# Performance work log

Hardware: AMD Instinct MI355X
Metric: run time of the kernel (lower is better)

## Reference

```python
import jax, jax.numpy as jnp
import numpy as np

B, M, LSEQ, D, K, H, DFF, NL = 16, 512, 1024, 128, 16, 8, 512, 2


def layernorm(x, g, b):
    mu = x.mean(-1, keepdims=True)
    var = ((x - mu) ** 2).mean(-1, keepdims=True)
    return (x - mu) * jax.lax.rsqrt(var + 1e-5) * g + b


def gcn_conv(x, row, col, W, b, N):
    # PyG GCNConv: xW, add self-loops, symmetric D^-1/2 (A+I) D^-1/2 aggregation
    xw = x @ W
    loop = jnp.arange(N)
    row2 = jnp.concatenate([row, loop])
    col2 = jnp.concatenate([col, loop])
    deg = jax.ops.segment_sum(jnp.ones(row2.shape[0], xw.dtype), col2, num_segments=N)
    dinv = jnp.where(deg > 0, jax.lax.rsqrt(deg), 0.0)
    norm = dinv[row2] * dinv[col2]  # [E+N]
    out = jax.ops.segment_sum(norm[:, None] * xw[row2], col2, num_segments=N)
    return out + b


def encoder_layer(q, kv, Wq, Wk, Wv, Wo, ln1_g, ln1_b, W1, b1, W2, b2, ln2_g, ln2_b):
    Bb, Mq, d = q.shape
    dh = d // H
    qh = (q @ Wq).reshape(Bb, Mq, H, dh)
    kh = (kv @ Wk).reshape(Bb, -1, H, dh)
    vh = (kv @ Wv).reshape(Bb, -1, H, dh)
    scores = jnp.einsum('bqhd,bkhd->bhqk', qh, kh) / jnp.sqrt(jnp.float32(dh))
    attn = jax.nn.softmax(scores, axis=-1)
    o = jnp.einsum('bhqk,bkhd->bqhd', attn, vh).reshape(Bb, Mq, d) @ Wo
    x = layernorm(q + o, ln1_g, ln1_b)
    ff = jax.nn.relu(x @ W1 + b1) @ W2 + b2
    return layernorm(x + ff, ln2_g, ln2_b)


def setup_inputs() -> dict:
    key = jax.random.key(0)
    ks = jax.random.split(key, 24)
    s = 0.05
    return {
        'enc_out_vari': jax.random.normal(ks[0], (B, M, D), jnp.float32),
        'x_enc': jax.random.normal(ks[1], (B, LSEQ, M), jnp.float32),
        'gcn_w1': jax.random.normal(ks[2], (D, D), jnp.float32) * s,
        'gcn_b1': jnp.zeros((D,), jnp.float32),
        'gcn_w2': jax.random.normal(ks[3], (D, D), jnp.float32) * s,
        'gcn_b2': jnp.zeros((D,), jnp.float32),
        'Wq': jax.random.normal(ks[4], (NL, D, D), jnp.float32) * s,
        'Wk': jax.random.normal(ks[5], (NL, D, D), jnp.float32) * s,
        'Wv': jax.random.normal(ks[6], (NL, D, D), jnp.float32) * s,
        'Wo': jax.random.normal(ks[7], (NL, D, D), jnp.float32) * s,
        'ln1_g': jnp.ones((NL, D), jnp.float32),
        'ln1_b': jnp.zeros((NL, D), jnp.float32),
        'W1': jax.random.normal(ks[8], (NL, D, DFF), jnp.float32) * s,
        'b1': jnp.zeros((NL, DFF), jnp.float32),
        'W2': jax.random.normal(ks[9], (NL, DFF, D), jnp.float32) * s,
        'b2': jnp.zeros((NL, D), jnp.float32),
        'ln2_g': jnp.ones((NL, D), jnp.float32),
        'ln2_b': jnp.zeros((NL, D), jnp.float32),
    }


def reference(enc_out_vari, x_enc, gcn_w1, gcn_b1, gcn_w2, gcn_b2, Wq, Wk, Wv, Wo,
              ln1_g, ln1_b, W1, b1, W2, b2, ln2_g, ln2_b):
    Bb, Mm, d = enc_out_vari.shape
    # --- Pearson correlation kNN graph build (ascending argsort as in source) ---
    xt = x_enc.transpose(0, 2, 1)  # [B, M, L]
    c = xt - xt.mean(-1, keepdims=True)
    cov = jnp.einsum('bml,bnl->bmn', c, c) / jnp.float32(LSEQ - 1)
    std = jnp.sqrt(jnp.diagonal(cov, axis1=-2, axis2=-1))
    std = jnp.where(std == 0, 1.0, std)
    corr = cov / (std[:, :, None] * std[:, None, :])
    neighbors = jnp.argsort(corr, axis=-1)[:, :, 1:K + 1]  # [B, M, K]
    # rows tiled, cols node-major (faithful to source's repeat/reshape mismatch)
    row = jnp.tile(jnp.arange(Mm), K)[None, :]           # [1, M*K]
    col = neighbors.reshape(Bb, -1)                      # [B, M*K]
    offs = (jnp.arange(Bb) * Mm)[:, None]
    row_g = jnp.broadcast_to(row + offs, (Bb, Mm * K)).reshape(-1)
    col_g = (col + offs).reshape(-1)
    N = Bb * Mm
    # --- 2-layer GCN on the disjoint-union graph (dropout is identity in eval) ---
    x_raw = enc_out_vari.reshape(N, d)
    x1 = jax.nn.relu(gcn_conv(x_raw, row_g, col_g, gcn_w1, gcn_b1, N))
    x2 = jax.nn.relu(gcn_conv(x1, row_g, col_g, gcn_w2, gcn_b2, N))
    kv = x2.reshape(Bb, Mm, d)
    # --- Transformer encoder: enc_out_vari attends to GCN features ---
    h = enc_out_vari
    for l in range(NL):
        h = encoder_layer(h, kv, Wq[l], Wk[l], Wv[l], Wo[l], ln1_g[l], ln1_b[l],
                          W1[l], b1[l], W2[l], b2[l], ln2_g[l], ln2_b[l])
    return h
```

## Files before the change

### kernel.cpp

```cpp
#include <hip/hip_runtime.h>
#include <math.h>

#define BB 16
#define MM 512
#define LL 1024
#define DD 128
#define KK 16
#define HH 8
#define DHH 16
#define NDFF 512
#define NNODE (BB*MM)
#define NEDGE (NNODE*KK)

typedef __attribute__((ext_vector_type(8))) short bf16x8;
typedef __attribute__((ext_vector_type(4))) float f32x4;
#define MFMA(a,b,c) __builtin_amdgcn_mfma_f32_16x16x32_bf16(a,b,c,0,0,0)

__device__ inline unsigned short bf16rne(float x) {
  union { float f; unsigned u; } v; v.f = x;
  return (unsigned short)((v.u + 0x7FFFu + ((v.u >> 16) & 1u)) >> 16);
}
__device__ inline float bf16tof(unsigned short h) {
  union { unsigned u; float f; } v; v.u = ((unsigned)h) << 16; return v.f;
}
__device__ inline void hilo(float x, unsigned short& h, unsigned short& l) {
  h = bf16rne(x);
  l = bf16rne(x - bf16tof(h));
}

__device__ inline void async16(const void* g, void* l) {
  __builtin_amdgcn_global_load_lds(
      (const __attribute__((address_space(1))) unsigned int*)g,
      (__attribute__((address_space(3))) unsigned int*)l, 16, 0, 0);
}

__global__ __launch_bounds__(256) void transpose_x_kernel(const float* __restrict__ X,
                                                          unsigned short* __restrict__ XTh,
                                                          unsigned short* __restrict__ XTl) {
  __shared__ float t[32][33];
  int b = blockIdx.z;
  int m0 = blockIdx.x * 32, l0 = blockIdx.y * 32;
  int c = threadIdx.x & 31, r = threadIdx.x >> 5;
  const float* Xb = X + (size_t)b * LL * MM;
  #pragma unroll
  for (int i = 0; i < 4; ++i)
    t[r + i*8][c] = Xb[(size_t)(l0 + r + i*8) * MM + m0 + c];
  __syncthreads();
  int R = m0 >> 6;
  int rbase = m0 & 63;
  size_t base = ((size_t)(b * 8 + R)) * 65536 + (size_t)(l0 >> 5) * 2048
              + (size_t)(c >> 3) * 512 + (c & 7);
  #pragma unroll
  for (int i = 0; i < 4; ++i) {
    unsigned short h, l;
    hilo(t[c][r + i*8], h, l);
    size_t idx = base + (size_t)(rbase + r + i*8) * 8;
    XTh[idx] = h; XTl[idx] = l;
  }
}

__global__ __launch_bounds__(256) void transpose_w_kernel(
    const float* __restrict__ gw1, const float* __restrict__ gw2,
    const float* __restrict__ Wq, const float* __restrict__ Wk,
    const float* __restrict__ Wv, const float* __restrict__ Wo,
    const float* __restrict__ W1, const float* __restrict__ W2,
    unsigned short* __restrict__ wTh, unsigned short* __restrict__ wTl) {
  int z = blockIdx.z;
  const float* src; int K, N; size_t doff;
  if (z < 10) {
    K = 128; N = 128;
    switch (z) {
      case 0: src = gw1;         doff = 0;         break;
      case 1: src = gw2;         doff = 16384;     break;
      case 2: src = Wk;          doff = 2*16384;   break;
      case 3: src = Wv;          doff = 3*16384;   break;
      case 4: src = Wk + 16384;  doff = 4*16384;   break;
      case 5: src = Wv + 16384;  doff = 5*16384;   break;
      case 6: src = Wq;          doff = 6*16384;   break;
      case 7: src = Wq + 16384;  doff = 7*16384;   break;
      case 8: src = Wo;          doff = 8*16384;   break;
      default: src = Wo + 16384; doff = 9*16384;   break;
    }
  } else if (z < 12) {
    K = 128; N = 512; doff = 163840 + (size_t)(z - 10) * 65536;
    src = W1 + (size_t)(z - 10) * 65536;
  } else {
    K = 512; N = 128; doff = 294912 + (size_t)(z - 12) * 65536;
    src = W2 + (size_t)(z - 12) * 65536;
  }
  int k0 = blockIdx.x * 32, n0 = blockIdx.y * 32;
  if (k0 >= K || n0 >= N) return;
  __shared__ float t[32][33];
  int c = threadIdx.x & 31, r = threadIdx.x >> 5;
  #pragma unroll
  for (int i = 0; i < 4; ++i)
    t[r + i*8][c] = src[(size_t)(k0 + r + i*8) * N + n0 + c];
  __syncthreads();
  #pragma unroll
  for (int i = 0; i < 4; ++i) {
    size_t idx = doff + (size_t)(n0 + r + i*8) * K + k0 + c;
    unsigned short h, l;
    hilo(t[c][r + i*8], h, l);
    wTh[idx] = h; wTl[idx] = l;
  }
}

__global__ void split_kernel(const float* __restrict__ in,
                             unsigned short* __restrict__ h,
                             unsigned short* __restrict__ l) {
  int i = blockIdx.x * 256 + threadIdx.x;
  float4 v = ((const float4*)in)[i];
  unsigned short h0,h1,h2,h3,l0,l1,l2,l3;
  hilo(v.x,h0,l0); hilo(v.y,h1,l1); hilo(v.z,h2,l2); hilo(v.w,h3,l3);
  uint2 hh, ll;
  hh.x = (unsigned)h0 | ((unsigned)h1 << 16); hh.y = (unsigned)h2 | ((unsigned)h3 << 16);
  ll.x = (unsigned)l0 | ((unsigned)l1 << 16); ll.y = (unsigned)l2 | ((unsigned)l3 << 16);
  ((uint2*)h)[i] = hh; ((uint2*)l)[i] = ll;
}

__global__ void colmean_part_kernel(const float* __restrict__ X, float* __restrict__ part) {
  int bm = blockIdx.x * 256 + threadIdx.x;
  int b = bm >> 9, m = bm & (MM - 1);
  int l0 = blockIdx.y * 128;
  const float* p = X + (size_t)b * LL * MM + (size_t)l0 * MM + m;
  float s = 0.f;
  #pragma unroll 8
  for (int l = 0; l < 128; ++l) s += p[(size_t)l * MM];
  part[(size_t)blockIdx.y * NNODE + bm] = s;
}

__global__ void colmean_finish_kernel(const float* __restrict__ part, float* __restrict__ mu) {
  int bm = blockIdx.x * 256 + threadIdx.x;
  float s = 0.f;
  #pragma unroll
  for (int j = 0; j < 8; ++j) s += part[(size_t)j * NNODE + bm];
  mu[bm] = s * (1.f / 1024.f);
}

__global__ __launch_bounds__(256) void gram_kernel(const unsigned short* __restrict__ XTh,
                                                   const unsigned short* __restrict__ XTl,
                                                   float* __restrict__ G0,
                                                   float* __restrict__ G1) {
  __shared__ unsigned short lAh[2048], lAl[2048], lBh[2048], lBl[2048];
  int b = blockIdx.y, z = blockIdx.z;
  int pi = blockIdx.x;
  int ti = 0, rem = pi;
  while (rem >= 8 - ti) { rem -= 8 - ti; ++ti; }
  int tj = ti + rem;
  int tid = threadIdx.x;
  int wid = tid >> 6, lane = tid & 63;
  int wr = wid >> 1, wc = wid & 1;
  int fr = lane & 15, fkb = lane >> 4;
  size_t abase = ((size_t)(b * 8 + ti)) * 65536 + (size_t)z * 16 * 2048;
  size_t bbase = ((size_t)(b * 8 + tj)) * 65536 + (size_t)z * 16 * 2048;
  int toff = tid * 8;
  int aoff0 = fkb * 512 + (wr*32 + fr) * 8;
  int aoff1 = aoff0 + 128;
  int boff0 = fkb * 512 + (wc*32 + fr) * 8;
  int boff1 = boff0 + 128;
  f32x4 acc00 = {0,0,0,0}, acc01 = {0,0,0,0}, acc10 = {0,0,0,0}, acc11 = {0,0,0,0};
  for (int s = 0; s < 16; ++s) {
    size_t ao = abase + (size_t)s * 2048 + toff;
    size_t bo = bbase + (size_t)s * 2048 + toff;
    async16(XTh + ao, lAh + toff);
    async16(XTl + ao, lAl + toff);
    async16(XTh + bo, lBh + toff);
    async16(XTl + bo, lBl + toff);
    __syncthreads();
    bf16x8 a0h = *(const bf16x8*)(lAh + aoff0);
    bf16x8 a1h = *(const bf16x8*)(lAh + aoff1);
    bf16x8 a0l = *(const bf16x8*)(lAl + aoff0);
    bf16x8 a1l = *(const bf16x8*)(lAl + aoff1);
    bf16x8 b0h = *(const bf16x8*)(lBh + boff0);
    bf16x8 b1h = *(const bf16x8*)(lBh + boff1);
    bf16x8 b0l = *(const bf16x8*)(lBl + boff0);
    bf16x8 b1l = *(const bf16x8*)(lBl + boff1);
    acc00 = MFMA(a0h, b0h, acc00); acc00 = MFMA(a0h, b0l, acc00); acc00 = MFMA(a0l, b0h, acc00);
    acc01 = MFMA(a0h, b1h, acc01); acc01 = MFMA(a0h, b1l, acc01); acc01 = MFMA(a0l, b1h, acc01);
    acc10 = MFMA(a1h, b0h, acc10); acc10 = MFMA(a1h, b0l, acc10); acc10 = MFMA(a1l, b0h, acc10);
    acc11 = MFMA(a1h, b1h, acc11); acc11 = MFMA(a1h, b1l, acc11); acc11 = MFMA(a1l, b1h, acc11);
    __syncthreads();
  }
  int m0 = ti * 64, n0 = tj * 64;
  float* G = (z ? G1 : G0) + (size_t)b * MM * MM;
  int mirror = (ti != tj);
  #pragma unroll
  for (int i = 0; i < 2; ++i) {
    #pragma unroll
    for (int j = 0; j < 2; ++j) {
      const f32x4& a = (i == 0) ? (j == 0 ? acc00 : acc01) : (j == 0 ? acc10 : acc11);
      #pragma unroll
      for (int r = 0; r < 4; ++r) {
        int row = m0 + wr*32 + i*16 + (lane >> 4)*4 + r;
        int col = n0 + wc*32 + j*16 + (lane & 15);
        float v = a[r];
        G[(size_t)row * MM + col] = v;
        if (mirror) G[(size_t)col * MM + row] = v;
      }
    }
  }
}

__global__ __launch_bounds__(256) void bf_gemm_k128_kernel(
    const unsigned short* __restrict__ Ah, const unsigned short* __restrict__ Al,
    const unsigned short* __restrict__ Bh, const unsigned short* __restrict__ Bl,
    float* __restrict__ C, unsigned short* __restrict__ Ch, unsigned short* __restrict__ Cl,
    int Ldc, int col0, const float* __restrict__ bias,
    const float* __restrict__ resid, int relu) {
  int tid = threadIdx.x;
  int m0 = blockIdx.y * 64, n0 = blockIdx.x * 64;
  int wid = tid >> 6, lane = tid & 63;
  int wr = wid >> 1, wc = wid & 1;
  int fr = lane & 15, fkb = lane >> 4;
  size_t arow0 = (size_t)(m0 + wr*32 + fr) * 128;
  size_t arow1 = arow0 + 16 * 128;
  size_t brow0 = (size_t)(n0 + wc*32 + fr) * 128;
  size_t brow1 = brow0 + 16 * 128;
  bf16x8 fa0h[4], fa1h[4], fa0l[4], fa1l[4];
  bf16x8 fb0h[4], fb1h[4], fb0l[4], fb1l[4];
  #pragma unroll
  for (int ks = 0; ks < 4; ++ks) {
    int ko = ks * 32 + fkb * 8;
    fa0h[ks] = *(const bf16x8*)(Ah + arow0 + ko);
    fa1h[ks] = *(const bf16x8*)(Ah + arow1 + ko);
    fa0l[ks] = *(const bf16x8*)(Al + arow0 + ko);
    fa1l[ks] = *(const bf16x8*)(Al + arow1 + ko);
    fb0h[ks] = *(const bf16x8*)(Bh + brow0 + ko);
    fb1h[ks] = *(const bf16x8*)(Bh + brow1 + ko);
    fb0l[ks] = *(const bf16x8*)(Bl + brow0 + ko);
    fb1l[ks] = *(const bf16x8*)(Bl + brow1 + ko);
  }
  f32x4 acc00 = {0,0,0,0}, acc01 = {0,0,0,0}, acc10 = {0,0,0,0}, acc11 = {0,0,0,0};
  #pragma unroll
  for (int ks = 0; ks < 4; ++ks) {
    acc00 = MFMA(fa0h[ks], fb0h[ks], acc00);
    acc00 = MFMA(fa0h[ks], fb0l[ks], acc00);
    acc00 = MFMA(fa0l[ks], fb0h[ks], acc00);
    acc01 = MFMA(fa0h[ks], fb1h[ks], acc01);
    acc01 = MFMA(fa0h[ks], fb1l[ks], acc01);
    acc01 = MFMA(fa0l[ks], fb1h[ks], acc01);
    acc10 = MFMA(fa1h[ks], fb0h[ks], acc10);
    acc10 = MFMA(fa1h[ks], fb0l[ks], acc10);
    acc10 = MFMA(fa1l[ks], fb0h[ks], acc10);
    acc11 = MFMA(fa1h[ks], fb1h[ks], acc11);
    acc11 = MFMA(fa1h[ks], fb1l[ks], acc11);
    acc11 = MFMA(fa1l[ks], fb1h[ks], acc11);
  }
  #pragma unroll
  for (int i = 0; i < 2; ++i) {
    #pragma unroll
    for (int j = 0; j < 2; ++j) {
      const f32x4& a = (i == 0) ? (j == 0 ? acc00 : acc01) : (j == 0 ? acc10 : acc11);
      #pragma unroll
      for (int r = 0; r < 4; ++r) {
        int row = m0 + wr*32 + i*16 + (lane >> 4)*4 + r;
        int col = col0 + n0 + wc*32 + j*16 + (lane & 15);
        float v = a[r];
        if (bias)  v += bias[col - col0];
        if (resid) v += resid[(size_t)row * Ldc + col];
        if (relu)  v = fmaxf(v, 0.f);
        size_t o = (size_t)row * Ldc + col;
        if (C) C[o] = v;
        if (Ch) {
          unsigned short hh, ll;
          hilo(v, hh, ll);
          Ch[o] = hh; Cl[o] = ll;
        }
      }
    }
  }
}

__global__ __launch_bounds__(512) void bf_gemm_sk_kernel(
    const unsigned short* __restrict__ Ah, const unsigned short* __restrict__ Al,
    const unsigned short* __restrict__ Bh, const unsigned short* __restrict__ Bl,
    float* __restrict__ C, unsigned short* __restrict__ Ch, unsigned short* __restrict__ Cl,
    int Ldc, int col0, int Kd, const float* __restrict__ bias,
    const float* __restrict__ resid, int relu) {
  __shared__ float red[64][65];
  int tid = threadIdx.x;
  int m0 = blockIdx.y * 64, n0 = blockIdx.x * 64;
  int wid = tid >> 6, lane = tid & 63;
  int kg = wid >> 2;
  int w4 = wid & 3;
  int wr = w4 >> 1, wc = w4 & 1;
  int fr = lane & 15, fkb = lane >> 4;
  int Kh = Kd >> 1;
  size_t arow0 = (size_t)(m0 + wr*32 + fr) * Kd + (size_t)kg * Kh;
  size_t arow1 = arow0 + (size_t)16 * Kd;
  size_t brow0 = (size_t)(n0 + wc*32 + fr) * Kd + (size_t)kg * Kh;
  size_t brow1 = brow0 + (size_t)16 * Kd;
  f32x4 acc00 = {0,0,0,0}, acc01 = {0,0,0,0}, acc10 = {0,0,0,0}, acc11 = {0,0,0,0};
  int ko = fkb * 8;
  bf16x8 a0h = *(const bf16x8*)(Ah + arow0 + ko);
  bf16x8 a1h = *(const bf16x8*)(Ah + arow1 + ko);
  bf16x8 a0l = *(const bf16x8*)(Al + arow0 + ko);
  bf16x8 a1l = *(const bf16x8*)(Al + arow1 + ko);
  bf16x8 b0h = *(const bf16x8*)(Bh + brow0 + ko);
  bf16x8 b1h = *(const bf16x8*)(Bh + brow1 + ko);
  bf16x8 b0l = *(const bf16x8*)(Bl + brow0 + ko);
  bf16x8 b1l = *(const bf16x8*)(Bl + brow1 + ko);
  for (int k0 = 32; k0 < Kh; k0 += 32) {
    int kn = k0 + fkb * 8;
    bf16x8 na0h = *(const bf16x8*)(Ah + arow0 + kn);
    bf16x8 na1h = *(const bf16x8*)(Ah + arow1 + kn);
    bf16x8 na0l = *(const bf16x8*)(Al + arow0 + kn);
    bf16x8 na1l = *(const bf16x8*)(Al + arow1 + kn);
    bf16x8 nb0h = *(const bf16x8*)(Bh + brow0 + kn);
    bf16x8 nb1h = *(const bf16x8*)(Bh + brow1 + kn);
    bf16x8 nb0l = *(const bf16x8*)(Bl + brow0 + kn);
    bf16x8 nb1l = *(const bf16x8*)(Bl + brow1 + kn);
    acc00 = MFMA(a0h, b0h, acc00); acc00 = MFMA(a0h, b0l, acc00); acc00 = MFMA(a0l, b0h, acc00);
    acc01 = MFMA(a0h, b1h, acc01); acc01 = MFMA(a0h, b1l, acc01); acc01 = MFMA(a0l, b1h, acc01);
    acc10 = MFMA(a1h, b0h, acc10); acc10 = MFMA(a1h, b0l, acc10); acc10 = MFMA(a1l, b0h, acc10);
    acc11 = MFMA(a1h, b1h, acc11); acc11 = MFMA(a1h, b1l, acc11); acc11 = MFMA(a1l, b1h, acc11);
    a0h = na0h; a1h = na1h; a0l = na0l; a1l = na1l;
    b0h = nb0h; b1h = nb1h; b0l = nb0l; b1l = nb1l;
  }
  acc00 = MFMA(a0h, b0h, acc00); acc00 = MFMA(a0h, b0l, acc00); acc00 = MFMA(a0l, b0h, acc00);
  acc01 = MFMA(a0h, b1h, acc01); acc01 = MFMA(a0h, b1l, acc01); acc01 = MFMA(a0l, b1h, acc01);
  acc10 = MFMA(a1h, b0h, acc10); acc10 = MFMA(a1h, b0l, acc10); acc10 = MFMA(a1l, b0h, acc10);
  acc11 = MFMA(a1h, b1h, acc11); acc11 = MFMA(a1h, b1l, acc11); acc11 = MFMA(a1l, b1h, acc11);
  if (kg == 1) {
    #pragma unroll
    for (int i = 0; i < 2; ++i) {
      #pragma unroll
      for (int j = 0; j < 2; ++j) {
        const f32x4& a = (i == 0) ? (j == 0 ? acc00 : acc01) : (j == 0 ? acc10 : acc11);
        #pragma unroll
        for (int r = 0; r < 4; ++r) {
          int lr = wr*32 + i*16 + (lane >> 4)*4 + r;
          int lc = wc*32 + j*16 + (lane & 15);
          red[lr][lc] = a[r];
        }
      }
    }
  }
  __syncthreads();
  if (kg == 0) {
    #pragma unroll
    for (int i = 0; i < 2; ++i) {
      #pragma unroll
      for (int j = 0; j < 2; ++j) {
        const f32x4& a = (i == 0) ? (j == 0 ? acc00 : acc01) : (j == 0 ? acc10 : acc11);
        #pragma unroll
        for (int r = 0; r < 4; ++r) {
          int lr = wr*32 + i*16 + (lane >> 4)*4 + r;
          int lc = wc*32 + j*16 + (lane & 15);
          int row = m0 + lr;
          int col = col0 + n0 + lc;
          float v = a[r] + red[lr][lc];
          if (bias)  v += bias[col - col0];
          if (resid) v += resid[(size_t)row * Ldc + col];
          if (relu)  v = fmaxf(v, 0.f);
          size_t o = (size_t)row * Ldc + col;
          if (C) C[o] = v;
          if (Ch) {
            unsigned short hh, ll;
            hilo(v, hh, ll);
            Ch[o] = hh; Cl[o] = ll;
          }
        }
      }
    }
  }
}

__global__ void rstd_kernel(const float* __restrict__ G0, const float* __restrict__ G1,
                            const float* __restrict__ mu, float* __restrict__ rstd) {
  int bm = blockIdx.x * 256 + threadIdx.x;
  int b = bm >> 9, m = bm & (MM - 1);
  size_t di = (size_t)b * MM * MM + (size_t)m * MM + m;
  float g = G0[di] + G1[di];
  float mm = mu[bm];
  float cov = (g - 1024.f * mm * mm) * (1.f / 1023.f);
  float sd = sqrtf(fmaxf(cov, 0.f));
  rstd[bm] = (sd == 0.f) ? 1.f : (1.f / sd);
}

__global__ void select_kernel(const float* __restrict__ G0, const float* __restrict__ G1,
                              const float* __restrict__ mu,
                              const float* __restrict__ rstd, int* __restrict__ nb) {
  int w = threadIdx.x >> 6, lane = threadIdx.x & 63;
  int bm = blockIdx.x * 4 + w;
  int b = bm >> 9, m = bm & (MM - 1);
  size_t rowoff = (size_t)b * MM * MM + (size_t)m * MM;
  const float* Gr0 = G0 + rowoff;
  const float* Gr1 = G1 + rowoff;
  const float* mub = mu + b * MM;
  const float* rsb = rstd + b * MM;
  float mm = mub[m], rm = rsb[m];
  float vals[8];
  int excl = 0;
  #pragma unroll
  for (int j = 0; j < 8; ++j) {
    int n = lane + j * 64;
    float cov = ((Gr0[n] + Gr1[n]) - 1024.f * mm * mub[n]) * (1.f / 1023.f);
    vals[j] = cov * rm * rsb[n];
  }
  int* out = nb + (size_t)bm * KK;
  for (int it = 0; it < KK + 1; ++it) {
    float bv = 1e30f; int bi = 1 << 30;
    #pragma unroll
    for (int j = 0; j < 8; ++j) {
      if (!((excl >> j) & 1)) {
        int n = lane + j * 64;
        if (vals[j] < bv) { bv = vals[j]; bi = n; }
      }
    }
    for (int off = 32; off; off >>= 1) {
      float v2 = __shfl_down(bv, off);
      int   i2 = __shfl_down(bi, off);
      if (v2 < bv || (v2 == bv && i2 < bi)) { bv = v2; bi = i2; }
    }
    bi = __shfl(bi, 0);
    if ((bi & 63) == lane) excl |= 1 << (bi >> 6);
    if (it > 0 && lane == 0) out[it - 1] = bi;
  }
}

__global__ void count_kernel(const int* __restrict__ nb, int* __restrict__ cnt) {
  int e = blockIdx.x * 256 + threadIdx.x;
  int b = e >> 13, i = e & 8191;
  int dst = b * MM + nb[(size_t)b * 8192 + i];
  atomicAdd(&cnt[dst], 1);
}

__global__ void scan_kernel(const int* __restrict__ cnt, int* __restrict__ offs,
                            int* __restrict__ curs, float* __restrict__ dinv) {
  __shared__ int part[256];
  int tid = threadIdx.x;
  int base = tid * 32;
  int local[32];
  int s = 0;
  #pragma unroll
  for (int i = 0; i < 32; ++i) { local[i] = cnt[base + i]; s += local[i]; }
  part[tid] = s;
  __syncthreads();
  for (int off = 1; off < 256; off <<= 1) {
    int v = (tid >= off) ? part[tid - off] : 0;
    __syncthreads();
    part[tid] += v;
    __syncthreads();
  }
  int run = part[tid] - s;
  #pragma unroll
  for (int i = 0; i < 32; ++i) {
    int n = base + i;
    offs[n] = run; curs[n] = run;
    run += local[i];
    dinv[n] = rsqrtf((float)(local[i] + 1));
  }
  if (tid == 255) offs[NNODE] = run;
}

__global__ void scatter_kernel(const int* __restrict__ nb, int* __restrict__ curs,
                               int* __restrict__ lists) {
  int e = blockIdx.x * 256 + threadIdx.x;
  int b = e >> 13, i = e & 8191;
  int dst = b * MM + nb[(size_t)b * 8192 + i];
  int src = b * MM + (i & (MM - 1));
  int pos = atomicAdd(&curs[dst], 1);
  lists[pos] = src;
}

__global__ void agg_kernel(const float* __restrict__ xw, const float* __restrict__ dinv,
                           const int* __restrict__ offs, const int* __restrict__ lists,
                           const float* __restrict__ bias,
                           unsigned short* __restrict__ outh,
                           unsigned short* __restrict__ outl) {
  int n = blockIdx.x * 2 + (threadIdx.x >> 7);
  int c = threadIdx.x & 127;
  float dn = dinv[n];
  float s = dn * xw[(size_t)n * DD + c];
  int e0 = offs[n], e1 = offs[n + 1];
  for (int e = e0; e < e1; ++e) {
    int src = lists[e];
    s += dinv[src] * xw[(size_t)src * DD + c];
  }
  float v = fmaxf(dn * s + bias[c], 0.f);
  unsigned short hh, ll;
  hilo(v, hh, ll);
  size_t o = (size_t)n * DD + c;
  outh[o] = hh; outl[o] = ll;
}

#define CH 128
#define KS(arr, r, j) arr[((r) << 4) + (((r) >> 5) << 3) + (j)]
__global__ __launch_bounds__(256) void attn_kernel(
    const float* __restrict__ Qb, const float* __restrict__ KVall, int ldkv, int kvoff,
    unsigned short* __restrict__ outh, unsigned short* __restrict__ outl) {
  __shared__ float ks[CH * 16 + 32];
  __shared__ float vs[CH * 16 + 32];
  int bx = blockIdx.x;
  int qc = bx & 7;
  int h  = (bx >> 3) & 7;
  int b  = bx >> 6;
  int tid = threadIdx.x;
  int r = tid >> 2;
  int p = tid & 3;
  int qrow = b * MM + qc * 64 + r;
  const float4* qp = (const float4*)(Qb + (size_t)qrow * DD + h * DHH);
  float4 q0 = qp[0], q1 = qp[1], q2 = qp[2], q3 = qp[3];
  float mval = -1e30f, l = 0.f;
  float4 o0 = {0,0,0,0}, o1 = {0,0,0,0}, o2 = {0,0,0,0}, o3 = {0,0,0,0};
  for (int ch = 0; ch < 4; ++ch) {
    __syncthreads();
    for (int idx = tid; idx < CH * 4; idx += 256) {
      int row = idx >> 2, seg = idx & 3;
      size_t kb = (size_t)(b * MM + ch * CH + row) * ldkv + kvoff + h * DHH + seg * 4;
      *(float4*)&KS(ks, row, seg * 4) = *(const float4*)&KVall[kb];
      *(float4*)&KS(vs, row, seg * 4) = *(const float4*)&KVall[kb + 128];
    }
    __syncthreads();
    #pragma unroll
    for (int t = 0; t < 2; ++t) {
      int kb = p * 32 + t * 16;
      float sc[16];
      #pragma unroll
      for (int kk = 0; kk < 16; ++kk) {
        float4 k0 = *(const float4*)&KS(ks, kb + kk, 0);
        float4 k1 = *(const float4*)&KS(ks, kb + kk, 4);
        float4 k2 = *(const float4*)&KS(ks, kb + kk, 8);
        float4 k3 = *(const float4*)&KS(ks, kb + kk, 12);
        float s = q0.x*k0.x + q0.y*k0.y + q0.z*k0.z + q0.w*k0.w
                + q1.x*k1.x + q1.y*k1.y + q1.z*k1.z + q1.w*k1.w
                + q2.x*k2.x + q2.y*k2.y + q2.z*k2.z + q2.w*k2.w
                + q3.x*k3.x + q3.y*k3.y + q3.z*k3.z + q3.w*k3.w;
        sc[kk] = s * 0.25f;
      }
      float tm = fmaxf(fmaxf(fmaxf(sc[0], sc[1]), fmaxf(sc[2], sc[3])),
                       fmaxf(fmaxf(sc[4], sc[5]), fmaxf(sc[6], sc[7])));
      tm = fmaxf(tm, fmaxf(fmaxf(fmaxf(sc[8], sc[9]), fmaxf(sc[10], sc[11])),
                           fmaxf(fmaxf(sc[12], sc[13]), fmaxf(sc[14], sc[15]))));
      float nm = fmaxf(mval, tm);
      float scale = __expf(mval - nm);
      float ls = 0.f;
      #pragma unroll
      for (int kk = 0; kk < 16; ++kk) { sc[kk] = __expf(sc[kk] - nm); ls += sc[kk]; }
      l = l * scale + ls;
      o0.x *= scale; o0.y *= scale; o0.z *= scale; o0.w *= scale;
      o1.x *= scale; o1.y *= scale; o1.z *= scale; o1.w *= scale;
      o2.x *= scale; o2.y *= scale; o2.z *= scale; o2.w *= scale;
      o3.x *= scale; o3.y *= scale; o3.z *= scale; o3.w *= scale;
      #pragma unroll
      for (int kk = 0; kk < 16; ++kk) {
        float wgt = sc[kk];
        float4 v0 = *(const float4*)&KS(vs, kb + kk, 0);
        float4 v1 = *(const float4*)&KS(vs, kb + kk, 4);
        float4 v2 = *(const float4*)&KS(vs, kb + kk, 8);
        float4 v3 = *(const float4*)&KS(vs, kb + kk, 12);
        o0.x += wgt*v0.x; o0.y += wgt*v0.y; o0.z += wgt*v0.z; o0.w += wgt*v0.w;
        o1.x += wgt*v1.x; o1.y += wgt*v1.y; o1.z += wgt*v1.z; o1.w += wgt*v1.w;
        o2.x += wgt*v2.x; o2.y += wgt*v2.y; o2.z += wgt*v2.z; o2.w += wgt*v2.w;
        o3.x += wgt*v3.x; o3.y += wgt*v3.y; o3.z += wgt*v3.z; o3.w += wgt*v3.w;
      }
      mval = nm;
    }
  }
  float o[16] = {o0.x,o0.y,o0.z,o0.w, o1.x,o1.y,o1.z,o1.w,
                 o2.x,o2.y,o2.z,o2.w, o3.x,o3.y,o3.z,o3.w};
  #pragma unroll
  for (int off = 1; off <= 2; off <<= 1) {
    float m2 = __shfl_xor(mval, off);
    float l2 = __shfl_xor(l, off);
    float nm = fmaxf(mval, m2);
    float s1 = __expf(mval - nm), s2 = __expf(m2 - nm);
    l = l * s1 + l2 * s2;
    #pragma unroll
    for (int j = 0; j < 16; ++j) {
      float o2v = __shfl_xor(o[j], off);
      o[j] = o[j] * s1 + o2v * s2;
    }
    mval = nm;
  }
  if (p == 0) {
    float invl = 1.f / l;
    size_t ob = (size_t)qrow * DD + h * DHH;
    #pragma unroll
    for (int j = 0; j < 16; ++j) {
      float v = o[j] * invl;
      unsigned short hh, ll;
      hilo(v, hh, ll);
      outh[ob + j] = hh; outl[ob + j] = ll;
    }
  }
}

__global__ void ln_kernel(const float* __restrict__ x, const float* __restrict__ g,
                          const float* __restrict__ bb, float* __restrict__ out,
                          unsigned short* __restrict__ outh,
                          unsigned short* __restrict__ outl) {
  int row = blockIdx.x * 4 + (threadIdx.x >> 6);
  int lane = threadIdx.x & 63;
  float2 xv = *(const float2*)&x[(size_t)row * DD + lane * 2];
  float s = xv.x + xv.y;
  #pragma unroll
  for (int off = 1; off < 64; off <<= 1) s += __shfl_xor(s, off);
  float mu = s * (1.f / 128.f);
  float d0 = xv.x - mu, d1 = xv.y - mu;
  float sq = d0 * d0 + d1 * d1;
  #pragma unroll
  for (int off = 1; off < 64; off <<= 1) sq += __shfl_xor(sq, off);
  float rs = rsqrtf(sq * (1.f / 128.f) + 1e-5f);
  float2 gg = *(const float2*)&g[lane * 2];
  float2 bv = *(const float2*)&bb[lane * 2];
  float2 y;
  y.x = d0 * rs * gg.x + bv.x;
  y.y = d1 * rs * gg.y + bv.y;
  *(float2*)&out[(size_t)row * DD + lane * 2] = y;
  if (outh) {
    unsigned short h0, l0, h1, l1;
    hilo(y.x, h0, l0); hilo(y.y, h1, l1);
    unsigned hh = (unsigned)h0 | ((unsigned)h1 << 16);
    unsigned ll = (unsigned)l0 | ((unsigned)l1 << 16);
    *(unsigned*)&outh[(size_t)row * DD + lane * 2] = hh;
    *(unsigned*)&outl[(size_t)row * DD + lane * 2] = ll;
  }
}

extern "C" void kernel_launch(void* const* d_in, const int* in_sizes, int n_in,
                              void* d_out, int out_size, void* d_ws, size_t ws_size,
                              hipStream_t stream) {
  (void)in_sizes; (void)n_in; (void)out_size; (void)ws_size;
  const float* enc  = (const float*)d_in[0];
  const float* xenc = (const float*)d_in[1];
  const float* gw1  = (const float*)d_in[2];
  const float* gb1  = (const float*)d_in[3];
  const float* gw2  = (const float*)d_in[4];
  const float* gb2  = (const float*)d_in[5];
  const float* Wq   = (const float*)d_in[6];
  const float* Wk   = (const float*)d_in[7];
  const float* Wv   = (const float*)d_in[8];
  const float* Wo   = (const float*)d_in[9];
  const float* ln1g = (const float*)d_in[10];
  const float* ln1b = (const float*)d_in[11];
  const float* W1   = (const float*)d_in[12];
  const float* b1   = (const float*)d_in[13];
  const float* W2   = (const float*)d_in[14];
  const float* b2   = (const float*)d_in[15];
  const float* ln2g = (const float*)d_in[16];
  const float* ln2b = (const float*)d_in[17];
  float* outp = (float*)d_out;

  char* w = (char*)d_ws;
  auto alloc = [&](size_t bytes) -> char* {
    char* p = w;
    w += (bytes + 255) & ~(size_t)255;
    return p;
  };
  float* mu    = (float*)alloc((size_t)NNODE * 4);
  float* rstd  = (float*)alloc((size_t)NNODE * 4);
  float* dinv  = (float*)alloc((size_t)NNODE * 4);
  float* mpart = (float*)alloc((size_t)8 * NNODE * 4);
  int*   nb    = (int*)  alloc((size_t)NEDGE * 4);
  int*   cnt   = (int*)  alloc((size_t)NNODE * 4);
  int*   offs  = (int*)  alloc((size_t)(NNODE + 1) * 4);
  int*   curs  = (int*)  alloc((size_t)NNODE * 4);
  int*   lists = (int*)  alloc((size_t)NEDGE * 4);
  float* gram  = (float*)alloc((size_t)BB * MM * MM * 4);
  float* gram2 = (float*)alloc((size_t)BB * MM * MM * 4);
  float* KVall = (float*)alloc((size_t)NNODE * 512 * 4);
  float* bufx  = (float*)alloc((size_t)NNODE * DD * 4);
  float* bufxl = (float*)alloc((size_t)NNODE * DD * 4);
  float* bufh  = (float*)alloc((size_t)NNODE * DD * 4);
  float* bufh1 = (float*)alloc((size_t)NNODE * DD * 4);
  unsigned short* xth  = (unsigned short*)alloc((size_t)BB * MM * LL * 2);
  unsigned short* xtl  = (unsigned short*)alloc((size_t)BB * MM * LL * 2);
  unsigned short* wTh  = (unsigned short*)alloc((size_t)425984 * 2);
  unsigned short* wTl  = (unsigned short*)alloc((size_t)425984 * 2);
  unsigned short* ench = (unsigned short*)alloc((size_t)NNODE * DD * 2);
  unsigned short* encl = (unsigned short*)alloc((size_t)NNODE * DD * 2);
  unsigned short* x1h  = (unsigned short*)alloc((size_t)NNODE * DD * 2);
  unsigned short* x1l  = (unsigned short*)alloc((size_t)NNODE * DD * 2);
  unsigned short* kvbh = (unsigned short*)alloc((size_t)NNODE * DD * 2);
  unsigned short* kvbl = (unsigned short*)alloc((size_t)NNODE * DD * 2);
  unsigned short* xlh  = (unsigned short*)alloc((size_t)NNODE * DD * 2);
  unsigned short* xll  = (unsigned short*)alloc((size_t)NNODE * DD * 2);
  unsigned short* h1h  = (unsigned short*)alloc((size_t)NNODE * DD * 2);
  unsigned short* h1l  = (unsigned short*)alloc((size_t)NNODE * DD * 2);
  unsigned short* sdh  = (unsigned short*)alloc((size_t)NNODE * DD * 2);
  unsigned short* sdl  = (unsigned short*)alloc((size_t)NNODE * DD * 2);

  float* Qb = gram;
  unsigned short* ffh = (unsigned short*)gram2;
  unsigned short* ffl = (unsigned short*)gram2 + (size_t)NNODE * NDFF;

  const unsigned short* gw1Th = wTh,         *gw1Tl = wTl;
  const unsigned short* gw2Th = wTh + 16384, *gw2Tl = wTl + 16384;
  const unsigned short* KVTh01 = wTh + (size_t)2 * 16384;
  const unsigned short* KVTl01 = wTl + (size_t)2 * 16384;
  auto WqTh = [&](int l) { return wTh + (size_t)(6 + l) * 16384; };
  auto WqTl = [&](int l) { return wTl + (size_t)(6 + l) * 16384; };
  auto WoTh = [&](int l) { return wTh + (size_t)(8 + l) * 16384; };
  auto WoTl = [&](int l) { return wTl + (size_t)(8 + l) * 16384; };
  auto W1Th = [&](int l) { return wTh + 163840 + (size_t)l * 65536; };
  auto W1Tl = [&](int l) { return wTl + 163840 + (size_t)l * 65536; };
  auto W2Th = [&](int l) { return wTh + 294912 + (size_t)l * 65536; };
  auto W2Tl = [&](int l) { return wTl + 294912 + (size_t)l * 65536; };

  auto gemm = [&](const unsigned short* Ah, const unsigned short* Al,
                  const unsigned short* Bh, const unsigned short* Bl,
                  float* C, unsigned short* Ch, unsigned short* Cl,
                  int Mr, int Ncols, int Ldc, int col0, int Kd,
                  const float* bias, const float* resid, int relu) {
    dim3 g(Ncols / 64, Mr / 64);
    if (Kd == 128) {
      bf_gemm_k128_kernel<<<g, 256, 0, stream>>>(Ah, Al, Bh, Bl, C, Ch, Cl, Ldc, col0,
                                                 bias, resid, relu);
    } else {
      bf_gemm_sk_kernel<<<g, 512, 0, stream>>>(Ah, Al, Bh, Bl, C, Ch, Cl, Ldc, col0, Kd,
                                               bias, resid, relu);
    }
  };

  transpose_x_kernel<<<dim3(16, 32, 16), 256, 0, stream>>>(xenc, xth, xtl);
  transpose_w_kernel<<<dim3(16, 16, 14), 256, 0, stream>>>(gw1, gw2, Wq, Wk, Wv, Wo, W1, W2, wTh, wTl);
  split_kernel<<<(NNODE * DD / 4) / 256, 256, 0, stream>>>(enc, ench, encl);

  colmean_part_kernel<<<dim3(32, 8), 256, 0, stream>>>(xenc, mpart);
  colmean_finish_kernel<<<NNODE / 256, 256, 0, stream>>>(mpart, mu);
  gram_kernel<<<dim3(36, BB, 2), 256, 0, stream>>>(xth, xtl, gram, gram2);
  rstd_kernel<<<NNODE / 256, 256, 0, stream>>>(gram, gram2, mu, rstd);
  select_kernel<<<NNODE / 4, 256, 0, stream>>>(gram, gram2, mu, rstd, nb);
  hipMemsetAsync(cnt, 0, (size_t)NNODE * 4, stream);
  count_kernel<<<NEDGE / 256, 256, 0, stream>>>(nb, cnt);
  scan_kernel<<<1, 256, 0, stream>>>(cnt, offs, curs, dinv);
  scatter_kernel<<<NEDGE / 256, 256, 0, stream>>>(nb, curs, lists);

  gemm(ench, encl, gw1Th, gw1Tl, bufx, nullptr, nullptr, NNODE, DD, DD, 0, DD,
       nullptr, nullptr, 0);
  agg_kernel<<<NNODE / 2, 256, 0, stream>>>(bufx, dinv, offs, lists, gb1, x1h, x1l);
  gemm(x1h, x1l, gw2Th, gw2Tl, bufx, nullptr, nullptr, NNODE, DD, DD, 0, DD,
       nullptr, nullptr, 0);
  agg_kernel<<<NNODE / 2, 256, 0, stream>>>(bufx, dinv, offs, lists, gb2, kvbh, kvbl);

  gemm(kvbh, kvbl, KVTh01, KVTl01, KVall, nullptr, nullptr, NNODE, 512, 512, 0, DD,
       nullptr, nullptr, 0);

  for (int l = 0; l < 2; ++l) {
    const float* hq = (l == 0) ? enc : bufh1;
    const unsigned short* hqh = (l == 0) ? ench : h1h;
    const unsigned short* hql = (l == 0) ? encl : h1l;
    gemm(hqh, hql, WqTh(l), WqTl(l), Qb, nullptr, nullptr, NNODE, DD, DD, 0, DD,
         nullptr, nullptr, 0);
    attn_kernel<<<BB * HH * 8, 256, 0, stream>>>(Qb, KVall, 512, l * 256, sdh, sdl);
    gemm(sdh, sdl, WoTh(l), WoTl(l), bufx, nullptr, nullptr, NNODE, DD, DD, 0, DD,
         nullptr, hq, 0);
    ln_kernel<<<NNODE / 4, 256, 0, stream>>>(bufx, ln1g + l * DD, ln1b + l * DD, bufxl, xlh, xll);
    gemm(xlh, xll, W1Th(l), W1Tl(l), nullptr, ffh, ffl, NNODE, NDFF, NDFF, 0, DD,
         b1 + l * NDFF, nullptr, 1);
    gemm(ffh, ffl, W2Th(l), W2Tl(l), bufh, nullptr, nullptr, NNODE, DD, DD, 0, NDFF,
         b2 + l * DD, bufxl, 0);
    if (l == 1) {
      ln_kernel<<<NNODE / 4, 256, 0, stream>>>(bufh, ln2g + l * DD, ln2b + l * DD,
                                               outp, nullptr, nullptr);
    } else {
      ln_kernel<<<NNODE / 4, 256, 0, stream>>>(bufh, ln2g + l * DD, ln2b + l * DD,
                                               bufh1, h1h, h1l);
    }
  }
}
```

Baseline: 445.6 us.

## Rewrite attention with bf16 MFMA and store Q/KV projections as bf16

Replaces the scalar fp32 flash-style attention kernel with one that computes QK^T and PV using bf16 16x16x32 MFMA instructions. The whole per-head K block and a transposed V block sit in shared memory, and probabilities are staged in LDS as bf16. The Q and KV projection GEMMs now write single bf16 outputs instead of fp32, which halves their memory traffic and removes the fp32 KV buffer. The cost is lower precision in Q, K, V and P, since these are single bf16 rather than hi/lo split or fp32, so accuracy could suffer. Half of each MFMA is zero-padded, because the head dim of 16 only fills half of the 32-wide k dimension.

```diff
diff --git a/kernel.cpp b/kernel.cpp
--- a/kernel.cpp
+++ b/kernel.cpp
@@ -262,9 +262,13 @@
         size_t o = (size_t)row * Ldc + col;
         if (C) C[o] = v;
         if (Ch) {
-          unsigned short hh, ll;
-          hilo(v, hh, ll);
-          Ch[o] = hh; Cl[o] = ll;
+          if (Cl) {
+            unsigned short hh, ll;
+            hilo(v, hh, ll);
+            Ch[o] = hh; Cl[o] = ll;
+          } else {
+            Ch[o] = bf16rne(v);
+          }
         }
       }
     }
@@ -485,105 +489,108 @@
   outh[o] = hh; outl[o] = ll;
 }
 
-#define CH 128
-#define KS(arr, r, j) arr[((r) << 4) + (((r) >> 5) << 3) + (j)]
-__global__ __launch_bounds__(256) void attn_kernel(
-    const float* __restrict__ Qb, const float* __restrict__ KVall, int ldkv, int kvoff,
+__global__ __launch_bounds__(256) void attn_mfma_kernel(
+    const unsigned short* __restrict__ Qb16, const unsigned short* __restrict__ KV16,
+    int kvoff,
     unsigned short* __restrict__ outh, unsigned short* __restrict__ outl) {
-  __shared__ float ks[CH * 16 + 32];
-  __shared__ float vs[CH * 16 + 32];
+  __shared__ unsigned short Kl[512 * 16];
+  __shared__ unsigned short VT[16 * 520];
+  __shared__ unsigned short Pl[64 * 136];
   int bx = blockIdx.x;
   int qc = bx & 7;
   int h  = (bx >> 3) & 7;
   int b  = bx >> 6;
   int tid = threadIdx.x;
-  int r = tid >> 2;
-  int p = tid & 3;
-  int qrow = b * MM + qc * 64 + r;
-  const float4* qp = (const float4*)(Qb + (size_t)qrow * DD + h * DHH);
-  float4 q0 = qp[0], q1 = qp[1], q2 = qp[2], q3 = qp[3];
-  float mval = -1e30f, l = 0.f;
-  float4 o0 = {0,0,0,0}, o1 = {0,0,0,0}, o2 = {0,0,0,0}, o3 = {0,0,0,0};
-  for (int ch = 0; ch < 4; ++ch) {
-    __syncthreads();
-    for (int idx = tid; idx < CH * 4; idx += 256) {
-      int row = idx >> 2, seg = idx & 3;
-      size_t kb = (size_t)(b * MM + ch * CH + row) * ldkv + kvoff + h * DHH + seg * 4;
-      *(float4*)&KS(ks, row, seg * 4) = *(const float4*)&KVall[kb];
-      *(float4*)&KS(vs, row, seg * 4) = *(const float4*)&KVall[kb + 128];
-    }
-    __syncthreads();
-    #pragma unroll
-    for (int t = 0; t < 2; ++t) {
-      int kb = p * 32 + t * 16;
-      float sc[16];
-      #pragma unroll
-      for (int kk = 0; kk < 16; ++kk) {
-        float4 k0 = *(const float4*)&KS(ks, kb + kk, 0);
-        float4 k1 = *(const float4*)&KS(ks, kb + kk, 4);
-        float4 k2 = *(const float4*)&KS(ks, kb + kk, 8);
-        float4 k3 = *(const float4*)&KS(ks, kb + kk, 12);
-        float s = q0.x*k0.x + q0.y*k0.y + q0.z*k0.z + q0.w*k0.w
-                + q1.x*k1.x + q1.y*k1.y + q1.z*k1.z + q1.w*k1.w
-                + q2.x*k2.x + q2.y*k2.y + q2.z*k2.z + q2.w*k2.w
-                + q3.x*k3.x + q3.y*k3.y + q3.z*k3.z + q3.w*k3.w;
-        sc[kk] = s * 0.25f;
-      }
-      float tm = fmaxf(fmaxf(fmaxf(sc[0], sc[1]), fmaxf(sc[2], sc[3])),
-                       fmaxf(fmaxf(sc[4], sc[5]), fmaxf(sc[6], sc[7])));
-      tm = fmaxf(tm, fmaxf(fmaxf(fmaxf(sc[8], sc[9]), fmaxf(sc[10], sc[11])),
-                           fmaxf(fmaxf(sc[12], sc[13]), fmaxf(sc[14], sc[15]))));
-      float nm = fmaxf(mval, tm);
-      float scale = __expf(mval - nm);
-      float ls = 0.f;
-      #pragma unroll
-      for (int kk = 0; kk < 16; ++kk) { sc[kk] = __expf(sc[kk] - nm); ls += sc[kk]; }
-      l = l * scale + ls;
-      o0.x *= scale; o0.y *= scale; o0.z *= scale; o0.w *= scale;
-      o1.x *= scale; o1.y *= scale; o1.z *= scale; o1.w *= scale;
-      o2.x *= scale; o2.y *= scale; o2.z *= scale; o2.w *= scale;
-      o3.x *= scale; o3.y *= scale; o3.z *= scale; o3.w *= scale;
-      #pragma unroll
-      for (int kk = 0; kk < 16; ++kk) {
-        float wgt = sc[kk];
-        float4 v0 = *(const float4*)&KS(vs, kb + kk, 0);
-        float4 v1 = *(const float4*)&KS(vs, kb + kk, 4);
-        float4 v2 = *(const float4*)&KS(vs, kb + kk, 8);
-        float4 v3 = *(const float4*)&KS(vs, kb + kk, 12);
-        o0.x += wgt*v0.x; o0.y += wgt*v0.y; o0.z += wgt*v0.z; o0.w += wgt*v0.w;
-        o1.x += wgt*v1.x; o1.y += wgt*v1.y; o1.z += wgt*v1.z; o1.w += wgt*v1.w;
-        o2.x += wgt*v2.x; o2.y += wgt*v2.y; o2.z += wgt*v2.z; o2.w += wgt*v2.w;
-        o3.x += wgt*v3.x; o3.y += wgt*v3.y; o3.z += wgt*v3.z; o3.w += wgt*v3.w;
-      }
-      mval = nm;
-    }
-  }
-  float o[16] = {o0.x,o0.y,o0.z,o0.w, o1.x,o1.y,o1.z,o1.w,
-                 o2.x,o2.y,o2.z,o2.w, o3.x,o3.y,o3.z,o3.w};
-  #pragma unroll
-  for (int off = 1; off <= 2; off <<= 1) {
-    float m2 = __shfl_xor(mval, off);
-    float l2 = __shfl_xor(l, off);
-    float nm = fmaxf(mval, m2);
-    float s1 = __expf(mval - nm), s2 = __expf(m2 - nm);
-    l = l * s1 + l2 * s2;
-    #pragma unroll
-    for (int j = 0; j < 16; ++j) {
-      float o2v = __shfl_xor(o[j], off);
-      o[j] = o[j] * s1 + o2v * s2;
-    }
-    mval = nm;
-  }
-  if (p == 0) {
-    float invl = 1.f / l;
-    size_t ob = (size_t)qrow * DD + h * DHH;
-    #pragma unroll
-    for (int j = 0; j < 16; ++j) {
-      float v = o[j] * invl;
-      unsigned short hh, ll;
-      hilo(v, hh, ll);
-      outh[ob + j] = hh; outl[ob + j] = ll;
-    }
+
+  for (int u = tid; u < 1024; u += 256) {
+    int row = u >> 1, half = u & 1;
+    const unsigned short* src = KV16 + (size_t)(b * MM + row) * 512 + kvoff + h * 16 + half * 8;
+    *(uint4*)&Kl[row * 16 + half * 8] = *(const uint4*)src;
+  }
+  for (int key = tid; key < 512; key += 256) {
+    const unsigned short* src = KV16 + (size_t)(b * MM + key) * 512 + kvoff + 128 + h * 16;
+    unsigned short tmp[16];
+    *(uint4*)&tmp[0] = *(const uint4*)src;
+    *(uint4*)&tmp[8] = *(const uint4*)(src + 8);
+    #pragma unroll
+    for (int d = 0; d < 16; ++d) VT[d * 520 + key] = tmp[d];
+  }
+  __syncthreads();
+
+  int wid = tid >> 6, lane = tid & 63;
+  int lq = lane & 15, g = lane >> 4;
+  bf16x8 zz = {0,0,0,0,0,0,0,0};
+  bf16x8 qf = zz;
+  if (lane < 32) {
+    int qrow = b * MM + qc * 64 + wid * 16 + lq;
+    qf = *(const bf16x8*)(Qb16 + (size_t)qrow * 128 + h * 16 + g * 8);
+  }
+  float m = -1e30f, lp = 0.f;
+  f32x4 o = {0,0,0,0};
+  int prow = (wid * 16 + lq) * 136;
+
+  for (int c4 = 0; c4 < 4; ++c4) {
+    int kbase = c4 * 128;
+    f32x4 s[8];
+    f32x4 zc = {0,0,0,0};
+    #pragma unroll
+    for (int t = 0; t < 8; ++t) {
+      bf16x8 kf = zz;
+      if (lane < 32) kf = *(const bf16x8*)&Kl[(kbase + t * 16 + lq) * 16 + g * 8];
+      s[t] = MFMA(kf, qf, zc);
+    }
+    float tm = -1e30f;
+    #pragma unroll
+    for (int t = 0; t < 8; ++t) {
+      tm = fmaxf(tm, fmaxf(fmaxf(s[t][0], s[t][1]), fmaxf(s[t][2], s[t][3])));
+    }
+    tm = fmaxf(tm, __shfl_xor(tm, 16));
+    tm = fmaxf(tm, __shfl_xor(tm, 32));
+    float nm = fmaxf(m, 0.25f * tm);
+    float esc = __expf(m - nm);
+    m = nm;
+    float ls = 0.f;
+    #pragma unroll
+    for (int t = 0; t < 8; ++t) {
+      float p0 = __expf(0.25f * s[t][0] - nm);
+      float p1 = __expf(0.25f * s[t][1] - nm);
+      float p2 = __expf(0.25f * s[t][2] - nm);
+      float p3 = __expf(0.25f * s[t][3] - nm);
+      ls += (p0 + p1) + (p2 + p3);
+      unsigned w0 = (unsigned)bf16rne(p0) | ((unsigned)bf16rne(p1) << 16);
+      unsigned w1 = (unsigned)bf16rne(p2) | ((unsigned)bf16rne(p3) << 16);
+      int kc = t * 16 + g * 4;
+      *(unsigned*)&Pl[prow + kc]     = w0;
+      *(unsigned*)&Pl[prow + kc + 2] = w1;
+    }
+    lp = lp * esc + ls;
+    float e0 = __shfl(esc, g * 4 + 0);
+    float e1 = __shfl(esc, g * 4 + 1);
+    float e2 = __shfl(esc, g * 4 + 2);
+    float e3 = __shfl(esc, g * 4 + 3);
+    o[0] *= e0; o[1] *= e1; o[2] *= e2; o[3] *= e3;
+    #pragma unroll
+    for (int c = 0; c < 4; ++c) {
+      bf16x8 pf = *(const bf16x8*)&Pl[prow + c * 32 + g * 8];
+      bf16x8 vf = *(const bf16x8*)&VT[lq * 520 + kbase + c * 32 + g * 8];
+      o = MFMA(pf, vf, o);
+    }
+  }
+  lp += __shfl_xor(lp, 16);
+  lp += __shfl_xor(lp, 32);
+  float linv = 1.f / lp;
+  float l0 = __shfl(linv, g * 4 + 0);
+  float l1 = __shfl(linv, g * 4 + 1);
+  float l2 = __shfl(linv, g * 4 + 2);
+  float l3 = __shfl(linv, g * 4 + 3);
+  float vv[4] = {o[0] * l0, o[1] * l1, o[2] * l2, o[3] * l3};
+  #pragma unroll
+  for (int r = 0; r < 4; ++r) {
+    int qrow = b * MM + qc * 64 + wid * 16 + g * 4 + r;
+    size_t off = (size_t)qrow * DD + h * 16 + lq;
+    unsigned short hh, ll;
+    hilo(vv[r], hh, ll);
+    outh[off] = hh; outl[off] = ll;
   }
 }
 
@@ -660,7 +667,6 @@
   int*   lists = (int*)  alloc((size_t)NEDGE * 4);
   float* gram  = (float*)alloc((size_t)BB * MM * MM * 4);
   float* gram2 = (float*)alloc((size_t)BB * MM * MM * 4);
-  float* KVall = (float*)alloc((size_t)NNODE * 512 * 4);
   float* bufx  = (float*)alloc((size_t)NNODE * DD * 4);
   float* bufxl = (float*)alloc((size_t)NNODE * DD * 4);
   float* bufh  = (float*)alloc((size_t)NNODE * DD * 4);
@@ -682,7 +688,8 @@
   unsigned short* sdh  = (unsigned short*)alloc((size_t)NNODE * DD * 2);
   unsigned short* sdl  = (unsigned short*)alloc((size_t)NNODE * DD * 2);
 
-  float* Qb = gram;
+  unsigned short* Qb16 = (unsigned short*)gram;
+  unsigned short* KV16 = (unsigned short*)(gram + (size_t)1048576);
   unsigned short* ffh = (unsigned short*)gram2;
   unsigned short* ffl = (unsigned short*)gram2 + (size_t)NNODE * NDFF;
 
@@ -735,16 +742,16 @@
        nullptr, nullptr, 0);
   agg_kernel<<<NNODE / 2, 256, 0, stream>>>(bufx, dinv, offs, lists, gb2, kvbh, kvbl);
 
-  gemm(kvbh, kvbl, KVTh01, KVTl01, KVall, nullptr, nullptr, NNODE, 512, 512, 0, DD,
+  gemm(kvbh, kvbl, KVTh01, KVTl01, nullptr, KV16, nullptr, NNODE, 512, 512, 0, DD,
        nullptr, nullptr, 0);
 
   for (int l = 0; l < 2; ++l) {
     const float* hq = (l == 0) ? enc : bufh1;
     const unsigned short* hqh = (l == 0) ? ench : h1h;
     const unsigned short* hql = (l == 0) ? encl : h1l;
-    gemm(hqh, hql, WqTh(l), WqTl(l), Qb, nullptr, nullptr, NNODE, DD, DD, 0, DD,
+    gemm(hqh, hql, WqTh(l), WqTl(l), nullptr, Qb16, nullptr, NNODE, DD, DD, 0, DD,
          nullptr, nullptr, 0);
-    attn_kernel<<<BB * HH * 8, 256, 0, stream>>>(Qb, KVall, 512, l * 256, sdh, sdl);
+    attn_mfma_kernel<<<BB * HH * 8, 256, 0, stream>>>(Qb16, KV16, l * 256, sdh, sdl);
     gemm(sdh, sdl, WoTh(l), WoTl(l), bufx, nullptr, nullptr, NNODE, DD, DD, 0, DD,
          nullptr, hq, 0);
     ln_kernel<<<NNODE / 4, 256, 0, stream>>>(bufx, ln1g + l * DD, ln1b + l * DD, bufxl, xlh, xll);
```

After: 390.0 us (median of 2 runs). 1.14x faster.
